# Optimization experiments

Measured on AMD Instinct MI355X. Metric: run time of the kernel, lower is better.

Reference implementation:

```python
import jax, jax.numpy as jnp
import numpy as np

N_NODES = 100000
N_EDGES = 1600000
ATOM_DIM = 16
POS_DIM = 3
HID = 128


def _linear_init(key, fan_in, fan_out):
    # torch nn.Linear default: U(-1/sqrt(fan_in), 1/sqrt(fan_in)) for W and b
    kw, kb = jax.random.split(key)
    bound = 1.0 / np.sqrt(fan_in)
    W = jax.random.uniform(kw, (fan_in, fan_out), jnp.float32, -bound, bound)
    b = jax.random.uniform(kb, (fan_out,), jnp.float32, -bound, bound)
    return W, b


def setup_inputs() -> dict:
    key = jax.random.key(0)
    ks = jax.random.split(key, 8)
    x = jax.random.normal(ks[0], (N_NODES, ATOM_DIM), jnp.float32)
    pos = jax.random.normal(ks[1], (N_NODES, POS_DIM), jnp.float32)
    edge_index = jax.random.randint(ks[2], (2, N_EDGES), 0, N_NODES, jnp.int64 if jax.config.jax_enable_x64 else jnp.int32)
    Wa, ba = _linear_init(ks[3], ATOM_DIM, HID)
    Wp, bp = _linear_init(ks[4], POS_DIM, HID)
    W1, b1 = _linear_init(ks[5], 2 * HID + 1, HID)
    W2, b2 = _linear_init(ks[6], HID, HID)
    W3, b3 = _linear_init(ks[7], HID, 4)
    return {"x": x, "pos": pos, "edge_index": edge_index,
            "Wa": Wa, "ba": ba, "Wp": Wp, "bp": bp,
            "W1": W1, "b1": b1, "W2": W2, "b2": b2, "W3": W3, "b3": b3}


def reference(x, pos, edge_index, Wa, ba, Wp, bp, W1, b1, W2, b2, W3, b3):
    # node embeddings: atom_emb + pos_emb, [N, HID]
    node_emb = (x @ Wa + ba) + (pos @ Wp + bp)
    src, dst = edge_index[0], edge_index[1]
    source_emb = node_emb[src]            # [E, HID]
    target_emb = node_emb[dst]            # [E, HID]
    diff = pos[src] - pos[dst]            # [E, 3]
    distances = jnp.linalg.norm(diff, axis=-1, keepdims=True)  # [E, 1]
    edge_input = jnp.concatenate([source_emb, target_emb, distances], axis=-1)  # [E, 2*HID+1]
    h = jax.nn.silu(edge_input @ W1 + b1)
    h = jax.nn.silu(h @ W2 + b2)
    bond_logits = h @ W3 + b3             # [E, 4]
    return bond_logits
```

## Files before the change

kernel.cpp:

```cpp
#include <hip/hip_runtime.h>
#include <hip/hip_bf16.h>
#include <hip/hip_fp16.h>

typedef _Float16 half8 __attribute__((ext_vector_type(8)));
typedef _Float16 half4 __attribute__((ext_vector_type(4)));
typedef __fp16 fp16x2 __attribute__((ext_vector_type(2)));
typedef float floatx4 __attribute__((ext_vector_type(4)));

#define HID 128
#define TILE_M 32

__device__ __forceinline__ float fast_silu(float v) {
    float e = __expf(-v);
    return v * __builtin_amdgcn_rcpf(1.f + e);
}

__device__ __forceinline__ unsigned int pk2(float a, float b) {
    fp16x2 h = __builtin_amdgcn_cvt_pkrtz(a, b);
    return __builtin_bit_cast(unsigned int, h);
}

#define LDO 136
__global__ __launch_bounds__(256) void node_emb_kernel(
    const float* __restrict__ x, const float* __restrict__ pos,
    const float* __restrict__ Wa, const float* __restrict__ ba,
    const float* __restrict__ Wp, const float* __restrict__ bp,
    _Float16* __restrict__ nodeEmb, int N)
{
    __shared__ __align__(16) _Float16 sOut[64 * LDO];
    const int t    = threadIdx.x;
    const int wave = t >> 6;
    const int lane = t & 63;
    const int quad = lane >> 4;
    const int l16  = lane & 15;

    half8 wf[2];
    floatx4 bias[2];
    #pragma unroll
    for (int ct = 0; ct < 2; ++ct) {
        int col = wave * 32 + ct * 16 + l16;
        #pragma unroll
        for (int j = 0; j < 8; ++j) {
            int k = quad * 8 + j;
            float w = 0.f;
            if (k < 16) w = Wa[k * HID + col];
            else if (k < 19) w = Wp[(k - 16) * HID + col];
            wf[ct][j] = (_Float16)w;
        }
        #pragma unroll
        for (int i = 0; i < 4; ++i) {
            int c2 = wave * 32 + ct * 16 + quad * 4 + i;
            bias[ct][i] = ba[c2] + bp[c2];
        }
    }

    int nTiles = (N + 63) >> 6;
    for (int tile = blockIdx.x; tile < nTiles; tile += gridDim.x) {
        int base = tile * 64;
        half8 af[4];
        #pragma unroll
        for (int rt = 0; rt < 4; ++rt) {
            int node = base + rt * 16 + l16;
            int nd = node < N ? node : N - 1;
            half8 a = (half8){0, 0, 0, 0, 0, 0, 0, 0};
            if (quad < 2) {
                const float* xp = x + (size_t)nd * 16 + quad * 8;
                float4 v0 = *(const float4*)xp;
                float4 v1 = *(const float4*)(xp + 4);
                a[0] = (_Float16)v0.x; a[1] = (_Float16)v0.y;
                a[2] = (_Float16)v0.z; a[3] = (_Float16)v0.w;
                a[4] = (_Float16)v1.x; a[5] = (_Float16)v1.y;
                a[6] = (_Float16)v1.z; a[7] = (_Float16)v1.w;
            } else if (quad == 2) {
                const float* pp = pos + (size_t)nd * 3;
                a[0] = (_Float16)pp[0]; a[1] = (_Float16)pp[1]; a[2] = (_Float16)pp[2];
            }
            af[rt] = a;
        }
        #pragma unroll
        for (int ct = 0; ct < 2; ++ct)
            #pragma unroll
            for (int rt = 0; rt < 4; ++rt) {
                floatx4 d = bias[ct];
                d = __builtin_amdgcn_mfma_f32_16x16x32_f16(wf[ct], af[rt], d, 0, 0, 0);
                half4 hv;
                hv[0] = (_Float16)d[0]; hv[1] = (_Float16)d[1];
                hv[2] = (_Float16)d[2]; hv[3] = (_Float16)d[3];
                *(half4*)&sOut[(rt * 16 + l16) * LDO + wave * 32 + ct * 16 + quad * 4] = hv;
            }
        __syncthreads();
        #pragma unroll
        for (int p = 0; p < 4; ++p) {
            int idx = p * 256 + t;
            int r = idx >> 4, c = idx & 15;
            int node = base + r;
            if (node < N)
                *(half8*)(nodeEmb + (size_t)node * HID + c * 8) =
                    *(const half8*)&sOut[r * LDO + c * 8];
        }
        __syncthreads();
    }
}

__global__ __launch_bounds__(512, 4) void edge_mlp_kernel(
    const _Float16* __restrict__ nodeEmb,
    const float* __restrict__ pos,
    const int* __restrict__ eidx,
    const float* __restrict__ W1, const float* __restrict__ b1,
    const float* __restrict__ W2, const float* __restrict__ b2,
    const float* __restrict__ W3, const float* __restrict__ b3,
    float* __restrict__ out, int E, int nTiles)
{
    __shared__ __align__(16) _Float16 sA[2 * TILE_M * HID];
    __shared__ __align__(16) _Float16 sH1[TILE_M * HID];
    __shared__ __align__(16) _Float16 sH2[TILE_M * HID];
    __shared__ float sDist[TILE_M];
    __shared__ __align__(16) _Float16 sW3[512];

    const int t    = threadIdx.x;
    const int wave = t >> 6;
    const int lane = t & 63;
    const int quad = lane >> 4;
    const int l16  = lane & 15;
    const int colbase = wave * 16;

    if (t < 64) {
        int kc = t >> 4, q = (t >> 2) & 3, c = t & 3;
        #pragma unroll
        for (int j = 0; j < 8; ++j)
            sW3[(kc * 16 + q * 4 + c) * 8 + j] =
                (_Float16)W3[(kc * 32 + q * 8 + j) * 4 + c];
    }

    half8 w1f[8];
    half8 w2f[4];
    float w1c[4], b1f[4], b2f[4];
    {
        int col = colbase + l16;
        #pragma unroll
        for (int kc = 0; kc < 8; ++kc)
            #pragma unroll
            for (int j = 0; j < 8; ++j)
                w1f[kc][j] = (_Float16)W1[(kc * 32 + quad * 8 + j) * HID + col];
        #pragma unroll
        for (int kc = 0; kc < 4; ++kc)
            #pragma unroll
            for (int j = 0; j < 8; ++j)
                w2f[kc][j] = (_Float16)W2[(kc * 32 + quad * 8 + j) * HID + col];
        #pragma unroll
        for (int i = 0; i < 4; ++i) {
            int c2 = colbase + quad * 4 + i;
            w1c[i] = W1[256 * HID + c2];
            b1f[i] = b1[c2];
            b2f[i] = b2[c2];
        }
    }
    const float b3v0 = b3[0], b3v1 = b3[1], b3v2 = b3[2], b3v3 = b3[3];

    int nid[2];
    float dpre = 0.f;

    auto load_nid = [&](int tl) {
        int eb = tl * TILE_M;
        #pragma unroll
        for (int i = 0; i < 2; ++i) {
            int cid = i * 512 + t;
            int row = cid >> 4;
            int r   = row & 31;
            int e   = eb + r; if (e >= E) e = E - 1;
            nid[i] = (row >> 5) ? eidx[(size_t)E + e] : eidx[e];
        }
    };
    auto load_dist = [&](int tl) -> float {
        if (t >= TILE_M) return 0.f;
        int e = tl * TILE_M + t; if (e >= E) e = E - 1;
        int s = eidx[e], d = eidx[(size_t)E + e];
        float dx = pos[3 * (size_t)s]     - pos[3 * (size_t)d];
        float dy = pos[3 * (size_t)s + 1] - pos[3 * (size_t)d + 1];
        float dz = pos[3 * (size_t)s + 2] - pos[3 * (size_t)d + 2];
        return sqrtf(dx * dx + dy * dy + dz * dz);
    };
    auto gather_issue = [&](half8 va[2]) {
        #pragma unroll
        for (int i = 0; i < 2; ++i) {
            int cid = i * 512 + t;
            int row = cid >> 4;
            int cg  = (cid & 15) ^ (row & 15);
            va[i] = *(const half8*)(nodeEmb + (size_t)nid[i] * HID + cg * 8);
        }
    };
    auto gather_write = [&](const half8 va[2]) {
        #pragma unroll
        for (int i = 0; i < 2; ++i) {
            int cid = i * 512 + t;
            *(half8*)&sA[cid * 8] = va[i];
        }
    };

    bool havePrev = false;
    int prevEbase = 0;
    int tile = blockIdx.x;
    if (tile < nTiles) {
        load_nid(tile);
        dpre = load_dist(tile);
        half8 va0[2];
        gather_issue(va0);
        gather_write(va0);
    }

    for (; tile < nTiles; tile += gridDim.x) {
        const int ebase = tile * TILE_M;
        if (t < TILE_M) sDist[t] = dpre;
        __syncthreads();

        if (havePrev && wave < 2) {
            floatx4 acc3 = (floatx4){0.f, 0.f, 0.f, 0.f};
            #pragma unroll
            for (int kc = 0; kc < 4; ++kc) {
                int slot = ((kc * 4 + quad) ^ l16) * 8;
                half8 h  = *(const half8*)&sH2[(wave * 16 + l16) * HID + slot];
                half8 w3 = *(const half8*)&sW3[(kc * 16 + quad * 4 + (l16 & 3)) * 8];
                acc3 = __builtin_amdgcn_mfma_f32_16x16x32_f16(w3, h, acc3, 0, 0, 0);
            }
            if (quad == 0) {
                int e = prevEbase + wave * 16 + l16;
                if (e < E) {
                    float4 o = {acc3[0] + b3v0, acc3[1] + b3v1,
                                acc3[2] + b3v2, acc3[3] + b3v3};
                    *(float4*)&out[(size_t)e * 4] = o;
                }
            }
        }

        int nxt = tile + gridDim.x;
        if (nxt < nTiles) {
            load_nid(nxt);
            dpre = load_dist(nxt);
        }

        floatx4 acc[2];
        #pragma unroll
        for (int rt = 0; rt < 2; ++rt) {
            acc[rt][0] = b1f[0]; acc[rt][1] = b1f[1];
            acc[rt][2] = b1f[2]; acc[rt][3] = b1f[3];
        }
        #pragma unroll
        for (int kc = 0; kc < 8; ++kc) {
            int hf   = kc >> 2;
            int cg   = (kc & 3) * 4 + quad;
            int slot = (cg ^ l16) * 8;
            const _Float16* base = &sA[(hf * TILE_M + l16) * HID + slot];
            half8 a0 = *(const half8*)(base + 0 * 16 * HID);
            half8 a1 = *(const half8*)(base + 1 * 16 * HID);
            acc[0] = __builtin_amdgcn_mfma_f32_16x16x32_f16(w1f[kc], a0, acc[0], 0, 0, 0);
            acc[1] = __builtin_amdgcn_mfma_f32_16x16x32_f16(w1f[kc], a1, acc[1], 0, 0, 0);
        }
        #pragma unroll
        for (int rt = 0; rt < 2; ++rt) {
            int m = rt * 16 + l16;
            float d = sDist[m];
            float v0 = fast_silu(fmaf(d, w1c[0], acc[rt][0]));
            float v1 = fast_silu(fmaf(d, w1c[1], acc[rt][1]));
            float v2 = fast_silu(fmaf(d, w1c[2], acc[rt][2]));
            float v3 = fast_silu(fmaf(d, w1c[3], acc[rt][3]));
            uint2 w;
            w.x = pk2(v0, v1);
            w.y = pk2(v2, v3);
            int cgb  = wave * 2 + (quad >> 1);
            int slot = cgb ^ l16;
            *(uint2*)&sH1[m * HID + slot * 8 + (quad & 1) * 4] = w;
        }
        __syncthreads();

        half8 va[2];
        if (nxt < nTiles) gather_issue(va);

        floatx4 acc2[2];
        #pragma unroll
        for (int rt = 0; rt < 2; ++rt) {
            acc2[rt][0] = b2f[0]; acc2[rt][1] = b2f[1];
            acc2[rt][2] = b2f[2]; acc2[rt][3] = b2f[3];
        }
        #pragma unroll
        for (int kc = 0; kc < 4; ++kc) {
            int slot = ((kc * 4 + quad) ^ l16) * 8;
            half8 a0 = *(const half8*)&sH1[(0 * 16 + l16) * HID + slot];
            half8 a1 = *(const half8*)&sH1[(1 * 16 + l16) * HID + slot];
            acc2[0] = __builtin_amdgcn_mfma_f32_16x16x32_f16(w2f[kc], a0, acc2[0], 0, 0, 0);
            acc2[1] = __builtin_amdgcn_mfma_f32_16x16x32_f16(w2f[kc], a1, acc2[1], 0, 0, 0);
        }

        if (nxt < nTiles) gather_write(va);

        #pragma unroll
        for (int rt = 0; rt < 2; ++rt) {
            int m = rt * 16 + l16;
            float v0 = fast_silu(acc2[rt][0]);
            float v1 = fast_silu(acc2[rt][1]);
            float v2 = fast_silu(acc2[rt][2]);
            float v3 = fast_silu(acc2[rt][3]);
            uint2 w;
            w.x = pk2(v0, v1);
            w.y = pk2(v2, v3);
            int cgb  = wave * 2 + (quad >> 1);
            int slot = cgb ^ l16;
            *(uint2*)&sH2[m * HID + slot * 8 + (quad & 1) * 4] = w;
        }
        havePrev = true;
        prevEbase = ebase;
    }

    if (havePrev) {
        __syncthreads();
        if (wave < 2) {
            floatx4 acc3 = (floatx4){0.f, 0.f, 0.f, 0.f};
            #pragma unroll
            for (int kc = 0; kc < 4; ++kc) {
                int slot = ((kc * 4 + quad) ^ l16) * 8;
                half8 h  = *(const half8*)&sH2[(wave * 16 + l16) * HID + slot];
                half8 w3 = *(const half8*)&sW3[(kc * 16 + quad * 4 + (l16 & 3)) * 8];
                acc3 = __builtin_amdgcn_mfma_f32_16x16x32_f16(w3, h, acc3, 0, 0, 0);
            }
            if (quad == 0) {
                int e = prevEbase + wave * 16 + l16;
                if (e < E) {
                    float4 o = {acc3[0] + b3v0, acc3[1] + b3v1,
                                acc3[2] + b3v2, acc3[3] + b3v3};
                    *(float4*)&out[(size_t)e * 4] = o;
                }
            }
        }
    }
}

extern "C" void kernel_launch(void* const* d_in, const int* in_sizes, int n_in,
                              void* d_out, int out_size, void* d_ws, size_t ws_size,
                              hipStream_t stream) {
    const float* x   = (const float*)d_in[0];
    const float* pos = (const float*)d_in[1];
    const int*  eidx = (const int*)d_in[2];
    const float* Wa = (const float*)d_in[3];
    const float* ba = (const float*)d_in[4];
    const float* Wp = (const float*)d_in[5];
    const float* bp = (const float*)d_in[6];
    const float* W1 = (const float*)d_in[7];
    const float* b1 = (const float*)d_in[8];
    const float* W2 = (const float*)d_in[9];
    const float* b2 = (const float*)d_in[10];
    const float* W3 = (const float*)d_in[11];
    const float* b3 = (const float*)d_in[12];
    float* out = (float*)d_out;

    int N = in_sizes[0] / 16;
    int E = in_sizes[2] / 2;

    _Float16* nodeEmb = (_Float16*)d_ws;

    int nodeTiles = (N + 63) / 64;
    node_emb_kernel<<<nodeTiles, 256, 0, stream>>>(x, pos, Wa, ba, Wp, bp, nodeEmb, N);

    int nTiles = (E + TILE_M - 1) / TILE_M;
    edge_mlp_kernel<<<1024, 512, 0, stream>>>(nodeEmb, pos, eidx,
                                              W1, b1, W2, b2, W3, b3,
                                              out, E, nTiles);
}
```

Before: 344.4 us.

## Stream pre-packed W2 fragments from global and move biases to LDS to cut registers

```diff
diff --git a/kernel.cpp b/kernel.cpp
--- a/kernel.cpp
+++ b/kernel.cpp
@@ -18,6 +18,17 @@
 __device__ __forceinline__ unsigned int pk2(float a, float b) {
     fp16x2 h = __builtin_amdgcn_cvt_pkrtz(a, b);
     return __builtin_bit_cast(unsigned int, h);
+}
+
+__global__ __launch_bounds__(256) void prep_w2_kernel(
+    const float* __restrict__ W2, _Float16* __restrict__ P)
+{
+    int idx = blockIdx.x * 256 + threadIdx.x;
+    if (idx >= 2048) return;
+    int q = idx & 3, c = (idx >> 2) & 127, kc = idx >> 9;
+    #pragma unroll
+    for (int j = 0; j < 8; ++j)
+        P[(size_t)idx * 8 + j] = (_Float16)W2[(kc * 32 + q * 8 + j) * HID + c];
 }
 
 #define LDO 136
@@ -104,6 +115,7 @@
 
 __global__ __launch_bounds__(512, 4) void edge_mlp_kernel(
     const _Float16* __restrict__ nodeEmb,
+    const _Float16* __restrict__ w2p,
     const float* __restrict__ pos,
     const int* __restrict__ eidx,
     const float* __restrict__ W1, const float* __restrict__ b1,
@@ -116,6 +128,9 @@
     __shared__ __align__(16) _Float16 sH2[TILE_M * HID];
     __shared__ float sDist[TILE_M];
     __shared__ __align__(16) _Float16 sW3[512];
+    __shared__ __align__(16) float sB1[HID];
+    __shared__ __align__(16) float sB2[HID];
+    __shared__ __align__(16) float sWc[HID];
 
     const int t    = threadIdx.x;
     const int wave = t >> 6;
@@ -131,10 +146,13 @@
             sW3[(kc * 16 + q * 4 + c) * 8 + j] =
                 (_Float16)W3[(kc * 32 + q * 8 + j) * 4 + c];
     }
+    if (t < HID) {
+        sB1[t] = b1[t];
+        sB2[t] = b2[t];
+        sWc[t] = W1[256 * HID + t];
+    }
 
     half8 w1f[8];
-    half8 w2f[4];
-    float w1c[4], b1f[4], b2f[4];
     {
         int col = colbase + l16;
         #pragma unroll
@@ -142,18 +160,6 @@
             #pragma unroll
             for (int j = 0; j < 8; ++j)
                 w1f[kc][j] = (_Float16)W1[(kc * 32 + quad * 8 + j) * HID + col];
-        #pragma unroll
-        for (int kc = 0; kc < 4; ++kc)
-            #pragma unroll
-            for (int j = 0; j < 8; ++j)
-                w2f[kc][j] = (_Float16)W2[(kc * 32 + quad * 8 + j) * HID + col];
-        #pragma unroll
-        for (int i = 0; i < 4; ++i) {
-            int c2 = colbase + quad * 4 + i;
-            w1c[i] = W1[256 * HID + c2];
-            b1f[i] = b1[c2];
-            b2f[i] = b2[c2];
-        }
     }
     const float b3v0 = b3[0], b3v1 = b3[1], b3v2 = b3[2], b3v3 = b3[3];
 
@@ -180,7 +186,8 @@
         float dz = pos[3 * (size_t)s + 2] - pos[3 * (size_t)d + 2];
         return sqrtf(dx * dx + dy * dy + dz * dz);
     };
-    auto gather_issue = [&](half8 va[2]) {
+    auto gather = [&]() {
+        half8 va[2];
         #pragma unroll
         for (int i = 0; i < 2; ++i) {
             int cid = i * 512 + t;
@@ -188,8 +195,6 @@
             int cg  = (cid & 15) ^ (row & 15);
             va[i] = *(const half8*)(nodeEmb + (size_t)nid[i] * HID + cg * 8);
         }
-    };
-    auto gather_write = [&](const half8 va[2]) {
         #pragma unroll
         for (int i = 0; i < 2; ++i) {
             int cid = i * 512 + t;
@@ -203,9 +208,7 @@
     if (tile < nTiles) {
         load_nid(tile);
         dpre = load_dist(tile);
-        half8 va0[2];
-        gather_issue(va0);
-        gather_write(va0);
+        gather();
     }
 
     for (; tile < nTiles; tile += gridDim.x) {
@@ -239,10 +242,9 @@
         }
 
         floatx4 acc[2];
-        #pragma unroll
-        for (int rt = 0; rt < 2; ++rt) {
-            acc[rt][0] = b1f[0]; acc[rt][1] = b1f[1];
-            acc[rt][2] = b1f[2]; acc[rt][3] = b1f[3];
+        {
+            floatx4 b1v = *(const floatx4*)&sB1[colbase + quad * 4];
+            acc[0] = b1v; acc[1] = b1v;
         }
         #pragma unroll
         for (int kc = 0; kc < 8; ++kc) {
@@ -255,43 +257,43 @@
             acc[0] = __builtin_amdgcn_mfma_f32_16x16x32_f16(w1f[kc], a0, acc[0], 0, 0, 0);
             acc[1] = __builtin_amdgcn_mfma_f32_16x16x32_f16(w1f[kc], a1, acc[1], 0, 0, 0);
         }
-        #pragma unroll
-        for (int rt = 0; rt < 2; ++rt) {
-            int m = rt * 16 + l16;
-            float d = sDist[m];
-            float v0 = fast_silu(fmaf(d, w1c[0], acc[rt][0]));
-            float v1 = fast_silu(fmaf(d, w1c[1], acc[rt][1]));
-            float v2 = fast_silu(fmaf(d, w1c[2], acc[rt][2]));
-            float v3 = fast_silu(fmaf(d, w1c[3], acc[rt][3]));
-            uint2 w;
-            w.x = pk2(v0, v1);
-            w.y = pk2(v2, v3);
-            int cgb  = wave * 2 + (quad >> 1);
-            int slot = cgb ^ l16;
-            *(uint2*)&sH1[m * HID + slot * 8 + (quad & 1) * 4] = w;
-        }
-        __syncthreads();
-
-        half8 va[2];
-        if (nxt < nTiles) gather_issue(va);
+        {
+            floatx4 w1cv = *(const floatx4*)&sWc[colbase + quad * 4];
+            #pragma unroll
+            for (int rt = 0; rt < 2; ++rt) {
+                int m = rt * 16 + l16;
+                float d = sDist[m];
+                float v0 = fast_silu(fmaf(d, w1cv[0], acc[rt][0]));
+                float v1 = fast_silu(fmaf(d, w1cv[1], acc[rt][1]));
+                float v2 = fast_silu(fmaf(d, w1cv[2], acc[rt][2]));
+                float v3 = fast_silu(fmaf(d, w1cv[3], acc[rt][3]));
+                uint2 w;
+                w.x = pk2(v0, v1);
+                w.y = pk2(v2, v3);
+                int cgb  = wave * 2 + (quad >> 1);
+                int slot = cgb ^ l16;
+                *(uint2*)&sH1[m * HID + slot * 8 + (quad & 1) * 4] = w;
+            }
+        }
+        __syncthreads();
+
+        if (nxt < nTiles) gather();
 
         floatx4 acc2[2];
-        #pragma unroll
-        for (int rt = 0; rt < 2; ++rt) {
-            acc2[rt][0] = b2f[0]; acc2[rt][1] = b2f[1];
-            acc2[rt][2] = b2f[2]; acc2[rt][3] = b2f[3];
+        {
+            floatx4 b2v = *(const floatx4*)&sB2[colbase + quad * 4];
+            acc2[0] = b2v; acc2[1] = b2v;
         }
         #pragma unroll
         for (int kc = 0; kc < 4; ++kc) {
+            half8 wc = *(const half8*)(w2p +
+                ((size_t)(kc * 128 + colbase + l16) * 4 + quad) * 8);
             int slot = ((kc * 4 + quad) ^ l16) * 8;
             half8 a0 = *(const half8*)&sH1[(0 * 16 + l16) * HID + slot];
             half8 a1 = *(const half8*)&sH1[(1 * 16 + l16) * HID + slot];
-            acc2[0] = __builtin_amdgcn_mfma_f32_16x16x32_f16(w2f[kc], a0, acc2[0], 0, 0, 0);
-            acc2[1] = __builtin_amdgcn_mfma_f32_16x16x32_f16(w2f[kc], a1, acc2[1], 0, 0, 0);
-        }
-
-        if (nxt < nTiles) gather_write(va);
-
+            acc2[0] = __builtin_amdgcn_mfma_f32_16x16x32_f16(wc, a0, acc2[0], 0, 0, 0);
+            acc2[1] = __builtin_amdgcn_mfma_f32_16x16x32_f16(wc, a1, acc2[1], 0, 0, 0);
+        }
         #pragma unroll
         for (int rt = 0; rt < 2; ++rt) {
             int m = rt * 16 + l16;
@@ -355,12 +357,15 @@
     int E = in_sizes[2] / 2;
 
     _Float16* nodeEmb = (_Float16*)d_ws;
+    _Float16* w2p = (_Float16*)((char*)d_ws + (size_t)N * HID * 2);
+
+    prep_w2_kernel<<<8, 256, 0, stream>>>(W2, w2p);
 
     int nodeTiles = (N + 63) / 64;
     node_emb_kernel<<<nodeTiles, 256, 0, stream>>>(x, pos, Wa, ba, Wp, bp, nodeEmb, N);
 
     int nTiles = (E + TILE_M - 1) / TILE_M;
-    edge_mlp_kernel<<<1024, 512, 0, stream>>>(nodeEmb, pos, eidx,
-                                              W1, b1, W2, b2, W3, b3,
-                                              out, E, nTiles);
-}
+    edge_mlp_kernel<<<768, 512, 0, stream>>>(nodeEmb, w2p, pos, eidx,
+                                             W1, b1, W2, b2, W3, b3,
+                                             out, E, nTiles);
+}
```

Measured after the change: 393.0 us. 1.14x slower.
